# Kernel tuning notes

Hardware: AMD Instinct MI355X
Metric: run time of the kernel (lower is better)

The kernel has to match this reference:

```python
import jax, jax.numpy as jnp
import numpy as np

B, S, L, H, C = 16, 2048, 256, 768, 512

def setup_inputs() -> dict:
    key = jax.random.key(0)
    ks = jax.random.split(key, 9)
    sc = 1.0 / np.sqrt(H)
    return {
        "input_hidden_states": jax.random.normal(ks[0], (B, S, H), jnp.float32),
        "label_hidden_states": jax.random.normal(ks[1], (L, H), jnp.float32),
        "Wi": jax.random.normal(ks[2], (C, H), jnp.float32) * sc,
        "bi": jnp.zeros((C,), jnp.float32),
        "Wl": jax.random.normal(ks[3], (C, H), jnp.float32) * sc,
        "bl": jnp.zeros((C,), jnp.float32),
        "Wia": jax.random.normal(ks[4], (C, H), jnp.float32) * sc,
        "bia": jnp.zeros((C,), jnp.float32),
        "Wla": jax.random.normal(ks[5], (C, H), jnp.float32) * sc,
        "bla": jnp.zeros((C,), jnp.float32),
        "context": jax.random.uniform(ks[6], (C,), jnp.float32),
        "Wp": jax.random.normal(ks[7], (H, C), jnp.float32) * (1.0 / np.sqrt(C)),
    }

def reference(input_hidden_states, label_hidden_states, Wi, bi, Wl, bl,
              Wia, bia, Wla, bla, context, Wp):
    # Dropout is identity in eval mode.
    x = input_hidden_states            # [B,S,H]
    lab = label_hidden_states          # [L,H] (original repeats over batch; math is identical)
    input_trans = jax.nn.sigmoid(jnp.einsum('bsh,ch->bsc', x, Wi) + bi)      # [B,S,C]
    label_trans = jax.nn.sigmoid(lab @ Wl.T + bl)                            # [L,C]
    input_attn = jax.nn.sigmoid(jnp.einsum('bsh,ch->bsc', x, Wia) + bia)    # [B,S,C]
    label_attn = jax.nn.sigmoid(lab @ Wla.T + bla)                          # [L,C]
    # attn logits: (context * input_attn) @ label_attn^T  -> [B,S,L]
    logits = jnp.einsum('bsc,lc->bsl', input_attn * context, label_attn)
    attn = jax.nn.softmax(logits, axis=-1)                                   # [B,S,L]
    # trilinear reduction: sum_{s,l} input_trans[b,s,c] * attn[b,s,l] * label_trans[l,c]
    weighted = jnp.einsum('bsl,lc->bsc', attn, label_trans)                  # [B,S,C]
    fusion = jnp.sum(input_trans * weighted, axis=1)                         # [B,C]
    return fusion @ Wp.T                                                     # [B,H]
```

## Files before the change

kernel.cpp:

```cpp
#include <hip/hip_runtime.h>

#define H_DIM 768
#define C_DIM 512
#define L_DIM 256
#define S_DIM 2048
#define B_DIM 16

#define IA_STRIDE 520
#define ATTN_STRIDE 264

typedef __attribute__((ext_vector_type(8))) short short8;
typedef __attribute__((ext_vector_type(4))) float f32x4;
typedef __attribute__((ext_vector_type(2))) __fp16 half2v;

#define MFMA_F16(a, b, c) __builtin_amdgcn_mfma_f32_16x16x32_f16((a), (b), (c), 0, 0, 0)

__device__ __forceinline__ unsigned short f2h(float f) {
    _Float16 h = (_Float16)f;
    return __builtin_bit_cast(unsigned short, h);
}
__device__ __forceinline__ float h2f(unsigned short u) {
    _Float16 h = __builtin_bit_cast(_Float16, u);
    return (float)h;
}
__device__ __forceinline__ float sigmoid_f(float x) { return 1.0f / (1.0f + __expf(-x)); }

__device__ __forceinline__ short8 cvt8(const float* p) {
    const float4* q = (const float4*)(const void*)p;
    float4 u = q[0], v = q[1];
    half2v h0 = __builtin_amdgcn_cvt_pkrtz(u.x, u.y);
    half2v h1 = __builtin_amdgcn_cvt_pkrtz(u.z, u.w);
    half2v h2 = __builtin_amdgcn_cvt_pkrtz(v.x, v.y);
    half2v h3 = __builtin_amdgcn_cvt_pkrtz(v.z, v.w);
    int4 pk = { __builtin_bit_cast(int, h0), __builtin_bit_cast(int, h1),
                __builtin_bit_cast(int, h2), __builtin_bit_cast(int, h3) };
    return __builtin_bit_cast(short8, pk);
}


__global__ __launch_bounds__(256) void prep_w(
    const float* __restrict__ Wi, const float* __restrict__ Wia,
    unsigned short* __restrict__ Wi_f, unsigned short* __restrict__ Wia_f)
{
    const int tid = blockIdx.x * 256 + threadIdx.x;
    const int m   = tid >= 49152;
    const int idx = tid - (m ? 49152 : 0);
    const int ct   = idx / 1536;
    const int rem  = idx - ct * 1536;
    const int kt   = rem >> 6;
    const int lane = rem & 63;
    const int row  = ct * 16 + (lane & 15);
    const int kcol = kt * 32 + (lane >> 4) * 8;
    const float* src = (m ? Wia : Wi) + (size_t)row * H_DIM + kcol;
    short8 v = cvt8(src);
    const int frag = ((ct >> 3) * 24 + kt) * 8 + (ct & 7);
    unsigned short* dst = (m ? Wia_f : Wi_f) + ((size_t)frag * 64 + lane) * 8;
    *(short8*)(void*)dst = v;
}

__global__ __launch_bounds__(256) void label_mfma(
    const float* __restrict__ lab,
    const float* __restrict__ Wl,  const float* __restrict__ bl,
    const float* __restrict__ Wla, const float* __restrict__ bla,
    const float* __restrict__ ctx,
    unsigned short* __restrict__ la_f,
    unsigned short* __restrict__ lt_f)
{
    const int tid  = threadIdx.x;
    const int wave = tid >> 6;
    const int lane = tid & 63;
    const int quad = lane >> 4;
    const int c16  = lane & 15;
    const int ct2  = blockIdx.x & 7;
    const int mh   = blockIdx.x >> 3;
    const int n0   = ct2 * 64 + wave * 16;
    const int l0   = mh * 32;

    const f32x4 z4 = {0.f, 0.f, 0.f, 0.f};
    f32x4 a1[2], a2[2];
#pragma unroll
    for (int mt = 0; mt < 2; ++mt) { a1[mt] = z4; a2[mt] = z4; }

    const float* lb  = lab + (size_t)(l0 + c16) * H_DIM + quad * 8;
    const float* wl  = Wl  + (size_t)(n0 + c16) * H_DIM + quad * 8;
    const float* wla = Wla + (size_t)(n0 + c16) * H_DIM + quad * 8;
    for (int kt = 0; kt < 24; ++kt) {
        const int kk = kt * 32;
        short8 b1 = cvt8(wl + kk);
        short8 b2 = cvt8(wla + kk);
#pragma unroll
        for (int mt = 0; mt < 2; ++mt) {
            short8 a = cvt8(lb + mt * 16 * H_DIM + kk);
            a1[mt] = MFMA_F16(a, b1, a1[mt]);
            a2[mt] = MFMA_F16(a, b2, a2[mt]);
        }
    }
    const int c = n0 + c16;
    const float blv = bl[c], blav = bla[c], cv = ctx[c];
#pragma unroll
    for (int mt = 0; mt < 2; ++mt)
#pragma unroll
        for (int r = 0; r < 4; ++r) {
            const int l = l0 + mt * 16 + quad * 4 + r;
            const float ltv = sigmoid_f(a1[mt][r] + blv);
            const float lav = sigmoid_f(a2[mt][r] + blav) * cv;
            {
                const int ct = c >> 4, ktl = l >> 5;
                const int frag = ((ct >> 3) * 8 + ktl) * 8 + (ct & 7);
                const int ln = (c & 15) | (((l >> 3) & 3) << 4);
                lt_f[((size_t)frag * 64 + ln) * 8 + (l & 7)] = f2h(ltv);
            }
            {
                const int lt = l >> 4, ktc = c >> 5;
                const int frag = ((lt >> 2) * 16 + ktc) * 4 + (lt & 3);
                const int ln = (l & 15) | (((c >> 3) & 3) << 4);
                la_f[((size_t)frag * 64 + ln) * 8 + (c & 7)] = f2h(lav);
            }
        }
}

__global__ __launch_bounds__(256, 4) void fused_main(
    const float* __restrict__ x,
    const float* __restrict__ bi,
    const float* __restrict__ bia,
    const unsigned short* __restrict__ Wi_f,
    const unsigned short* __restrict__ Wia_f,
    const unsigned short* __restrict__ lt_f,
    const unsigned short* __restrict__ la_f,
    float* __restrict__ fusion)
{
    __shared__ unsigned short lds_buf[32 * IA_STRIDE];
    __shared__ float rowscratch[4 * 32];
    __shared__ float inv_lds[32];

    const int tid  = threadIdx.x;
    const int wave = tid >> 6;
    const int lane = tid & 63;
    const int quad = lane >> 4;
    const int c16  = lane & 15;

    const int row0 = blockIdx.x * 32;
    const int b    = row0 >> 11;

    const f32x4 z4 = {0.f, 0.f, 0.f, 0.f};
    const int n0 = wave * 128;

    const float* xb = x + (size_t)(row0 + c16) * H_DIM + quad * 8;

    {
        f32x4 acc[2][8];
#pragma unroll
        for (int mt = 0; mt < 2; ++mt)
#pragma unroll
            for (int nt = 0; nt < 8; ++nt) acc[mt][nt] = z4;
        const short8* wa8 = (const short8*)(const void*)Wia_f + (size_t)wave * 192 * 64 + lane;
        for (int kt = 0; kt < 24; ++kt) {
            short8 a0 = cvt8(xb + kt * 32);
            short8 a1 = cvt8(xb + 16 * H_DIM + kt * 32);
#pragma unroll
            for (int nt = 0; nt < 8; ++nt) {
                short8 ba = wa8[(kt * 8 + nt) * 64];
                acc[0][nt] = MFMA_F16(a0, ba, acc[0][nt]);
                acc[1][nt] = MFMA_F16(a1, ba, acc[1][nt]);
            }
        }
#pragma unroll
        for (int nt = 0; nt < 8; ++nt) {
            const int col = n0 + nt * 16 + c16;
            const float bv = bia[col];
#pragma unroll
            for (int mt = 0; mt < 2; ++mt)
#pragma unroll
                for (int r = 0; r < 4; ++r) {
                    const int row = mt * 16 + quad * 4 + r;
                    lds_buf[row * IA_STRIDE + col] = f2h(sigmoid_f(acc[mt][nt][r] + bv));
                }
        }
    }
    __syncthreads();

    const int n0l = wave * 64;
    f32x4 accl[2][4];
#pragma unroll
    for (int mt = 0; mt < 2; ++mt)
#pragma unroll
        for (int nt = 0; nt < 4; ++nt) accl[mt][nt] = z4;
    {
        const unsigned short* ab = lds_buf + c16 * IA_STRIDE + quad * 8;
        const short8* la8 = (const short8*)(const void*)la_f + (size_t)wave * 64 * 64 + lane;
        for (int kt = 0; kt < 16; ++kt) {
            const int kk = kt * 32;
            short8 a0 = *(const short8*)(const void*)(ab + kk);
            short8 a1 = *(const short8*)(const void*)(ab + 16 * IA_STRIDE + kk);
#pragma unroll
            for (int nt = 0; nt < 4; ++nt) {
                short8 bfr = la8[(kt * 4 + nt) * 64];
                accl[0][nt] = MFMA_F16(a0, bfr, accl[0][nt]);
                accl[1][nt] = MFMA_F16(a1, bfr, accl[1][nt]);
            }
        }
    }
    __syncthreads();

    float rmax[2][4];
#pragma unroll
    for (int mt = 0; mt < 2; ++mt)
#pragma unroll
        for (int r = 0; r < 4; ++r) {
            float m = accl[mt][0][r];
#pragma unroll
            for (int nt = 1; nt < 4; ++nt) m = fmaxf(m, accl[mt][nt][r]);
#pragma unroll
            for (int off = 1; off < 16; off <<= 1) m = fmaxf(m, __shfl_xor(m, off, 64));
            rmax[mt][r] = m;
        }
    if (c16 == 0) {
#pragma unroll
        for (int mt = 0; mt < 2; ++mt)
#pragma unroll
            for (int r = 0; r < 4; ++r)
                rowscratch[wave * 32 + mt * 16 + quad * 4 + r] = rmax[mt][r];
    }
    __syncthreads();
    float rsum[2][4];
#pragma unroll
    for (int mt = 0; mt < 2; ++mt)
#pragma unroll
        for (int r = 0; r < 4; ++r) {
            const int row = mt * 16 + quad * 4 + r;
            float gm = rowscratch[row];
#pragma unroll
            for (int w = 1; w < 4; ++w) gm = fmaxf(gm, rowscratch[w * 32 + row]);
            float s = 0.f;
#pragma unroll
            for (int nt = 0; nt < 4; ++nt) {
                float e = __expf(accl[mt][nt][r] - gm);
                accl[mt][nt][r] = e;
                s += e;
            }
#pragma unroll
            for (int off = 1; off < 16; off <<= 1) s += __shfl_xor(s, off, 64);
            rsum[mt][r] = s;
        }
    __syncthreads();
    if (c16 == 0) {
#pragma unroll
        for (int mt = 0; mt < 2; ++mt)
#pragma unroll
            for (int r = 0; r < 4; ++r)
                rowscratch[wave * 32 + mt * 16 + quad * 4 + r] = rsum[mt][r];
    }
    __syncthreads();
#pragma unroll
    for (int mt = 0; mt < 2; ++mt)
#pragma unroll
        for (int r = 0; r < 4; ++r) {
            const int row = mt * 16 + quad * 4 + r;
            const float st = rowscratch[row] + rowscratch[32 + row]
                           + rowscratch[64 + row] + rowscratch[96 + row];
            if (wave == 0 && c16 == 0) inv_lds[row] = 1.0f / st;
#pragma unroll
            for (int nt = 0; nt < 4; ++nt)
                lds_buf[row * ATTN_STRIDE + n0l + nt * 16 + c16] = f2h(accl[mt][nt][r]);
        }
    __syncthreads();

    f32x4 accw[2][8];
#pragma unroll
    for (int mt = 0; mt < 2; ++mt)
#pragma unroll
        for (int nt = 0; nt < 8; ++nt) accw[mt][nt] = z4;
    {
        const unsigned short* ab = lds_buf + c16 * ATTN_STRIDE + quad * 8;
        const short8* lt8 = (const short8*)(const void*)lt_f + (size_t)wave * 64 * 64 + lane;
        for (int kt = 0; kt < 8; ++kt) {
            const int kk = kt * 32;
            short8 a0 = *(const short8*)(const void*)(ab + kk);
            short8 a1 = *(const short8*)(const void*)(ab + 16 * ATTN_STRIDE + kk);
#pragma unroll
            for (int nt = 0; nt < 8; ++nt) {
                short8 bfr = lt8[(kt * 8 + nt) * 64];
                accw[0][nt] = MFMA_F16(a0, bfr, accw[0][nt]);
                accw[1][nt] = MFMA_F16(a1, bfr, accw[1][nt]);
            }
        }
    }
    __syncthreads();

    {
        float invr[2][4];
#pragma unroll
        for (int mt = 0; mt < 2; ++mt)
#pragma unroll
            for (int r = 0; r < 4; ++r) invr[mt][r] = inv_lds[mt * 16 + quad * 4 + r];
#pragma unroll
        for (int nt = 0; nt < 8; ++nt) {
            const int col = n0 + nt * 16 + c16;
#pragma unroll
            for (int mt = 0; mt < 2; ++mt)
#pragma unroll
                for (int r = 0; r < 4; ++r) {
                    const int row = mt * 16 + quad * 4 + r;
                    lds_buf[row * IA_STRIDE + col] = f2h(accw[mt][nt][r] * invr[mt][r]);
                }
        }
    }

    {
        f32x4 acc[2][8];
#pragma unroll
        for (int mt = 0; mt < 2; ++mt)
#pragma unroll
            for (int nt = 0; nt < 8; ++nt) acc[mt][nt] = z4;
        const short8* wi8 = (const short8*)(const void*)Wi_f + (size_t)wave * 192 * 64 + lane;
        for (int kt = 0; kt < 24; ++kt) {
            short8 a0 = cvt8(xb + kt * 32);
            short8 a1 = cvt8(xb + 16 * H_DIM + kt * 32);
#pragma unroll
            for (int nt = 0; nt < 8; ++nt) {
                short8 bw = wi8[(kt * 8 + nt) * 64];
                acc[0][nt] = MFMA_F16(a0, bw, acc[0][nt]);
                acc[1][nt] = MFMA_F16(a1, bw, acc[1][nt]);
            }
        }
#pragma unroll
        for (int nt = 0; nt < 8; ++nt) {
            const int col = n0 + nt * 16 + c16;
            const float bv = bi[col];
            float s = 0.f;
#pragma unroll
            for (int mt = 0; mt < 2; ++mt)
#pragma unroll
                for (int r = 0; r < 4; ++r) {
                    const int row = mt * 16 + quad * 4 + r;
                    s += h2f(lds_buf[row * IA_STRIDE + col]) * sigmoid_f(acc[mt][nt][r] + bv);
                }
            s += __shfl_xor(s, 16, 64);
            s += __shfl_xor(s, 32, 64);
            if (lane < 16) atomicAdd(&fusion[b * C_DIM + col], s);
        }
    }
}

__global__ __launch_bounds__(256) void out_kernel(
    const float* __restrict__ fusion,
    const float* __restrict__ Wp,
    float* __restrict__ out)
{
    const int idx = blockIdx.x * 256 + threadIdx.x;
    const int R   = idx >> 3;
    const int sub = idx & 7;
    const int bb  = R / H_DIM;
    const int h   = R - bb * H_DIM;
    const float* wp = Wp + (size_t)h * C_DIM;
    const float* f  = fusion + bb * C_DIM;
    float s = 0.f;
#pragma unroll
    for (int j = 0; j < 16; ++j) {
        const int c = j * 32 + sub * 4;
        float4 wv = *(const float4*)(const void*)(wp + c);
        float4 fv = *(const float4*)(const void*)(f + c);
        s += fv.x * wv.x + fv.y * wv.y + fv.z * wv.z + fv.w * wv.w;
    }
    s += __shfl_xor(s, 1, 64);
    s += __shfl_xor(s, 2, 64);
    s += __shfl_xor(s, 4, 64);
    if (sub == 0) out[R] = s;
}

extern "C" void kernel_launch(void* const* d_in, const int* in_sizes, int n_in,
                              void* d_out, int out_size, void* d_ws, size_t ws_size,
                              hipStream_t stream)
{
    const float* x    = (const float*)d_in[0];
    const float* lab  = (const float*)d_in[1];
    const float* Wi   = (const float*)d_in[2];
    const float* bi   = (const float*)d_in[3];
    const float* Wl   = (const float*)d_in[4];
    const float* bl   = (const float*)d_in[5];
    const float* Wia  = (const float*)d_in[6];
    const float* bia  = (const float*)d_in[7];
    const float* Wla  = (const float*)d_in[8];
    const float* bla  = (const float*)d_in[9];
    const float* ctx  = (const float*)d_in[10];
    const float* Wp   = (const float*)d_in[11];

    char* ws = (char*)d_ws;
    unsigned short* Wi_f  = (unsigned short*)(ws);
    unsigned short* Wia_f = (unsigned short*)(ws + 786432);
    unsigned short* la_f  = (unsigned short*)(ws + 1572864);
    unsigned short* lt_f  = (unsigned short*)(ws + 1835008);
    float* fusion         = (float*)(ws + 2097152);

    (void)hipMemsetAsync(fusion, 0, B_DIM * C_DIM * sizeof(float), stream);
    prep_w<<<384, 256, 0, stream>>>(Wi, Wia, Wi_f, Wia_f);
    label_mfma<<<64, 256, 0, stream>>>(lab, Wl, bl, Wla, bla, ctx, la_f, lt_f);
    fused_main<<<(B_DIM * S_DIM) / 32, 256, 0, stream>>>(x, bi, bia, Wi_f, Wia_f, lt_f, la_f, fusion);
    out_kernel<<<384, 256, 0, stream>>>(fusion, Wp, (float*)d_out);
}
```

Measured before the change: 349.8 us.

## Pre-convert x and label weights to fp16 MFMA fragment layout

Adds a prep_x kernel that converts the fp32 input activations once into fp16 fragment-ordered tiles, so fused_main reads half the bytes and skips the per-load conversion, which it previously did twice (once per GEMM). prep_w also pre-packs Wl and Wla so label_mfma reads fragments directly. In exchange, an extra full pass over x (read fp32, write fp16) is added, plus a larger workspace requirement; if the workspace is too small it falls back to the old path.

```diff
diff --git a/kernel.cpp b/kernel.cpp
--- a/kernel.cpp
+++ b/kernel.cpp
@@ -40,28 +40,44 @@
 
 __global__ __launch_bounds__(256) void prep_w(
     const float* __restrict__ Wi, const float* __restrict__ Wia,
-    unsigned short* __restrict__ Wi_f, unsigned short* __restrict__ Wia_f)
+    const float* __restrict__ Wl, const float* __restrict__ Wla,
+    unsigned short* __restrict__ Wi_f, unsigned short* __restrict__ Wia_f,
+    unsigned short* __restrict__ Wl_f, unsigned short* __restrict__ Wla_f)
 {
     const int tid = blockIdx.x * 256 + threadIdx.x;
-    const int m   = tid >= 49152;
-    const int idx = tid - (m ? 49152 : 0);
+    const int m   = tid / 49152;
+    const int idx = tid - m * 49152;
     const int ct   = idx / 1536;
     const int rem  = idx - ct * 1536;
     const int kt   = rem >> 6;
     const int lane = rem & 63;
     const int row  = ct * 16 + (lane & 15);
     const int kcol = kt * 32 + (lane >> 4) * 8;
-    const float* src = (m ? Wia : Wi) + (size_t)row * H_DIM + kcol;
-    short8 v = cvt8(src);
+    const float* src = (m == 0 ? Wi : (m == 1 ? Wia : (m == 2 ? Wl : Wla)));
+    unsigned short* dst = (m == 0 ? Wi_f : (m == 1 ? Wia_f : (m == 2 ? Wl_f : Wla_f)));
+    short8 v = cvt8(src + (size_t)row * H_DIM + kcol);
     const int frag = ((ct >> 3) * 24 + kt) * 8 + (ct & 7);
-    unsigned short* dst = (m ? Wia_f : Wi_f) + ((size_t)frag * 64 + lane) * 8;
-    *(short8*)(void*)dst = v;
+    *(short8*)(void*)(dst + ((size_t)frag * 64 + lane) * 8) = v;
+}
+
+__global__ __launch_bounds__(256) void prep_x(
+    const float* __restrict__ x, unsigned short* __restrict__ x_f)
+{
+    const int tid = blockIdx.x * 256 + threadIdx.x;
+    const int mt  = tid / 1536;
+    const int rem = tid - mt * 1536;
+    const int kt  = rem >> 6;
+    const int lane = rem & 63;
+    const int row = mt * 16 + (lane & 15);
+    const int col = kt * 32 + (lane >> 4) * 8;
+    short8 v = cvt8(x + (size_t)row * H_DIM + col);
+    *(short8*)(void*)(x_f + ((size_t)(mt * 24 + kt) * 64 + lane) * 8) = v;
 }
 
 __global__ __launch_bounds__(256) void label_mfma(
     const float* __restrict__ lab,
-    const float* __restrict__ Wl,  const float* __restrict__ bl,
-    const float* __restrict__ Wla, const float* __restrict__ bla,
+    const unsigned short* __restrict__ Wl_f,  const float* __restrict__ bl,
+    const unsigned short* __restrict__ Wla_f, const float* __restrict__ bla,
     const float* __restrict__ ctx,
     unsigned short* __restrict__ la_f,
     unsigned short* __restrict__ lt_f)
@@ -73,7 +89,8 @@
     const int c16  = lane & 15;
     const int ct2  = blockIdx.x & 7;
     const int mh   = blockIdx.x >> 3;
-    const int n0   = ct2 * 64 + wave * 16;
+    const int ct   = ct2 * 4 + wave;
+    const int n0   = ct * 16;
     const int l0   = mh * 32;
 
     const f32x4 z4 = {0.f, 0.f, 0.f, 0.f};
@@ -81,16 +98,15 @@
 #pragma unroll
     for (int mt = 0; mt < 2; ++mt) { a1[mt] = z4; a2[mt] = z4; }
 
-    const float* lb  = lab + (size_t)(l0 + c16) * H_DIM + quad * 8;
-    const float* wl  = Wl  + (size_t)(n0 + c16) * H_DIM + quad * 8;
-    const float* wla = Wla + (size_t)(n0 + c16) * H_DIM + quad * 8;
+    const float* lb = lab + (size_t)(l0 + c16) * H_DIM + quad * 8;
+    const short8* wl8  = (const short8*)(const void*)Wl_f  + ((size_t)(ct >> 3) * 24 * 8 + (ct & 7)) * 64 + lane;
+    const short8* wla8 = (const short8*)(const void*)Wla_f + ((size_t)(ct >> 3) * 24 * 8 + (ct & 7)) * 64 + lane;
     for (int kt = 0; kt < 24; ++kt) {
-        const int kk = kt * 32;
-        short8 b1 = cvt8(wl + kk);
-        short8 b2 = cvt8(wla + kk);
+        short8 b1 = wl8[kt * 8 * 64];
+        short8 b2 = wla8[kt * 8 * 64];
 #pragma unroll
         for (int mt = 0; mt < 2; ++mt) {
-            short8 a = cvt8(lb + mt * 16 * H_DIM + kk);
+            short8 a = cvt8(lb + mt * 16 * H_DIM + kt * 32);
             a1[mt] = MFMA_F16(a, b1, a1[mt]);
             a2[mt] = MFMA_F16(a, b2, a2[mt]);
         }
@@ -105,8 +121,8 @@
             const float ltv = sigmoid_f(a1[mt][r] + blv);
             const float lav = sigmoid_f(a2[mt][r] + blav) * cv;
             {
-                const int ct = c >> 4, ktl = l >> 5;
-                const int frag = ((ct >> 3) * 8 + ktl) * 8 + (ct & 7);
+                const int ctc = c >> 4, ktl = l >> 5;
+                const int frag = ((ctc >> 3) * 8 + ktl) * 8 + (ctc & 7);
                 const int ln = (c & 15) | (((l >> 3) & 3) << 4);
                 lt_f[((size_t)frag * 64 + ln) * 8 + (l & 7)] = f2h(ltv);
             }
@@ -119,7 +135,9 @@
         }
 }
 
+template<bool XF>
 __global__ __launch_bounds__(256, 4) void fused_main(
+    const unsigned short* __restrict__ x_f,
     const float* __restrict__ x,
     const float* __restrict__ bi,
     const float* __restrict__ bia,
@@ -145,7 +163,8 @@
     const f32x4 z4 = {0.f, 0.f, 0.f, 0.f};
     const int n0 = wave * 128;
 
-    const float* xb = x + (size_t)(row0 + c16) * H_DIM + quad * 8;
+    const float*  xb  = x + (size_t)(row0 + c16) * H_DIM + quad * 8;
+    const short8* xf8 = (const short8*)(const void*)x_f + ((size_t)blockIdx.x * 2 * 24) * 64 + lane;
 
     {
         f32x4 acc[2][8];
@@ -155,8 +174,9 @@
             for (int nt = 0; nt < 8; ++nt) acc[mt][nt] = z4;
         const short8* wa8 = (const short8*)(const void*)Wia_f + (size_t)wave * 192 * 64 + lane;
         for (int kt = 0; kt < 24; ++kt) {
-            short8 a0 = cvt8(xb + kt * 32);
-            short8 a1 = cvt8(xb + 16 * H_DIM + kt * 32);
+            short8 a0, a1;
+            if constexpr (XF) { a0 = xf8[kt * 64]; a1 = xf8[(24 + kt) * 64]; }
+            else { a0 = cvt8(xb + kt * 32); a1 = cvt8(xb + 16 * H_DIM + kt * 32); }
 #pragma unroll
             for (int nt = 0; nt < 8; ++nt) {
                 short8 ba = wa8[(kt * 8 + nt) * 64];
@@ -314,8 +334,9 @@
             for (int nt = 0; nt < 8; ++nt) acc[mt][nt] = z4;
         const short8* wi8 = (const short8*)(const void*)Wi_f + (size_t)wave * 192 * 64 + lane;
         for (int kt = 0; kt < 24; ++kt) {
-            short8 a0 = cvt8(xb + kt * 32);
-            short8 a1 = cvt8(xb + 16 * H_DIM + kt * 32);
+            short8 a0, a1;
+            if constexpr (XF) { a0 = xf8[kt * 64]; a1 = xf8[(24 + kt) * 64]; }
+            else { a0 = cvt8(xb + kt * 32); a1 = cvt8(xb + 16 * H_DIM + kt * 32); }
 #pragma unroll
             for (int nt = 0; nt < 8; ++nt) {
                 short8 bw = wi8[(kt * 8 + nt) * 64];
@@ -388,13 +409,24 @@
     char* ws = (char*)d_ws;
     unsigned short* Wi_f  = (unsigned short*)(ws);
     unsigned short* Wia_f = (unsigned short*)(ws + 786432);
-    unsigned short* la_f  = (unsigned short*)(ws + 1572864);
-    unsigned short* lt_f  = (unsigned short*)(ws + 1835008);
-    float* fusion         = (float*)(ws + 2097152);
+    unsigned short* Wl_f  = (unsigned short*)(ws + 1572864);
+    unsigned short* Wla_f = (unsigned short*)(ws + 2359296);
+    unsigned short* la_f  = (unsigned short*)(ws + 3145728);
+    unsigned short* lt_f  = (unsigned short*)(ws + 3407872);
+    float* fusion         = (float*)(ws + 3670016);
+    unsigned short* x_f   = (unsigned short*)(ws + 3702784);
+    const size_t NEED_XF  = 3702784 + (size_t)32768 * 768 * 2;
 
     (void)hipMemsetAsync(fusion, 0, B_DIM * C_DIM * sizeof(float), stream);
-    prep_w<<<384, 256, 0, stream>>>(Wi, Wia, Wi_f, Wia_f);
-    label_mfma<<<64, 256, 0, stream>>>(lab, Wl, bl, Wla, bla, ctx, la_f, lt_f);
-    fused_main<<<(B_DIM * S_DIM) / 32, 256, 0, stream>>>(x, bi, bia, Wi_f, Wia_f, lt_f, la_f, fusion);
+    prep_w<<<768, 256, 0, stream>>>(Wi, Wia, Wl, Wla, Wi_f, Wia_f, Wl_f, Wla_f);
+    label_mfma<<<64, 256, 0, stream>>>(lab, Wl_f, bl, Wla_f, bla, ctx, la_f, lt_f);
+    if (ws_size >= NEED_XF) {
+        prep_x<<<12288, 256, 0, stream>>>(x, x_f);
+        fused_main<true><<<(B_DIM * S_DIM) / 32, 256, 0, stream>>>(
+            x_f, x, bi, bia, Wi_f, Wia_f, lt_f, la_f, fusion);
+    } else {
+        fused_main<false><<<(B_DIM * S_DIM) / 32, 256, 0, stream>>>(
+            nullptr, x, bi, bia, Wi_f, Wia_f, lt_f, la_f, fusion);
+    }
     out_kernel<<<384, 256, 0, stream>>>(fusion, Wp, (float*)d_out);
 }
```

Measured after the change: 332.4 us. -5.0%, faster.
